# Performance work log

Hardware: AMD Instinct MI355X
Metric: run time of the kernel (lower is better)

## Reference

```python
import jax, jax.numpy as jnp
import numpy as np

L, H, D, DH, F, V, S, B, CTX = 6, 12, 768, 64, 3072, 32000, 1024, 2, 1024
EPS = 1e-5


def layernorm(x, scale, bias):
    mu = jnp.mean(x, axis=-1, keepdims=True)
    var = jnp.mean(jnp.square(x - mu), axis=-1, keepdims=True)
    return (x - mu) * jax.lax.rsqrt(var + EPS) * scale + bias


def setup_inputs() -> dict:
    key = jax.random.key(0)
    ks = jax.random.split(key, 16)
    std = 0.02
    res_std = 0.02 * (2 * L) ** (-0.5)
    inp = {
        "X": jax.random.randint(ks[0], (B, S), 0, V),
        "emb": jax.random.normal(ks[1], (V, D), jnp.float32) * std,            # tied with head weight
        "pos_emb": jax.random.normal(ks[2], (CTX, D), jnp.float32) * 0.01,
        "Wq": jax.random.normal(ks[3], (L, H, D, DH), jnp.float32) * std,
        "bq": jnp.zeros((L, H, DH), jnp.float32),
        "Wk": jax.random.normal(ks[4], (L, H, D, DH), jnp.float32) * std,
        "bk": jnp.zeros((L, H, DH), jnp.float32),
        "Wv": jax.random.normal(ks[5], (L, H, D, DH), jnp.float32) * std,
        "bv": jnp.zeros((L, H, DH), jnp.float32),
        "Wo": jax.random.normal(ks[6], (L, H * DH, D), jnp.float32) * res_std,  # ResidualScaledLinear
        "bo": jnp.zeros((L, D), jnp.float32),
        "ln1_s": jnp.ones((L, D), jnp.float32),
        "ln1_b": jnp.zeros((L, D), jnp.float32),
        "ln2_s": jnp.ones((L, D), jnp.float32),
        "ln2_b": jnp.zeros((L, D), jnp.float32),
        "W1": jax.random.normal(ks[7], (L, D, F), jnp.float32) * std,
        "b1": jnp.zeros((L, F), jnp.float32),
        "W2": jax.random.normal(ks[8], (L, F, D), jnp.float32) * res_std,       # ResidualScaledLinear
        "b2": jnp.zeros((L, D), jnp.float32),
        "lnf_s": jnp.ones((D,), jnp.float32),
        "lnf_b": jnp.zeros((D,), jnp.float32),
        "head_b": jnp.zeros((V,), jnp.float32),
    }
    return inp


def decoder_forward(X, emb, pos_emb, Wq, bq, Wk, bk, Wv, bv, Wo, bo,
                    ln1_s, ln1_b, ln2_s, ln2_b, W1, b1, W2, b2,
                    lnf_s, lnf_b, head_b):
    seq = X.shape[1]
    x = emb[X] + pos_emb[:seq]                      # [B,S,D]
    causal = jnp.tril(jnp.ones((seq, seq), bool))   # tril mask buffer
    scale = 1.0 / jnp.sqrt(jnp.float32(DH))
    for l in range(L):
        xn = layernorm(x, ln1_s[l], ln1_b[l])
        q = jnp.einsum('bsd,hdk->bhsk', xn, Wq[l]) + bq[l][None, :, None, :]
        k = jnp.einsum('bsd,hdk->bhsk', xn, Wk[l]) + bk[l][None, :, None, :]
        v = jnp.einsum('bsd,hdk->bhsk', xn, Wv[l]) + bv[l][None, :, None, :]
        scores = jnp.einsum('bhsk,bhtk->bhst', q, k) * scale
        scores = jnp.where(causal, scores, -jnp.inf)
        attn = jax.nn.softmax(scores, axis=-1)
        out = jnp.einsum('bhst,bhtk->bshk', attn, v).reshape(x.shape[0], seq, H * DH)
        x = x + out @ Wo[l] + bo[l]
        xn2 = layernorm(x, ln2_s[l], ln2_b[l])
        x = x + jax.nn.relu(xn2 @ W1[l] + b1[l]) @ W2[l] + b2[l]
    x = layernorm(x, lnf_s, lnf_b)
    return x @ emb.T + head_b                       # tied head weight


def reference(X, emb, pos_emb, Wq, bq, Wk, bk, Wv, bv, Wo, bo,
              ln1_s, ln1_b, ln2_s, ln2_b, W1, b1, W2, b2,
              lnf_s, lnf_b, head_b):
    return decoder_forward(X, emb, pos_emb, Wq, bq, Wk, bk, Wv, bv, Wo, bo,
                           ln1_s, ln1_b, ln2_s, ln2_b, W1, b1, W2, b2,
                           lnf_s, lnf_b, head_b)
```

## Files before the change

kernel.cpp:

```cpp
#include <hip/hip_runtime.h>
#include <cstdint>
#include <cstddef>

#define CL 6
#define CH 12
#define CD 768
#define CDH 64
#define CF 3072
#define CV 32000
#define CS 1024
#define CB 2
#define CM (CB*CS)
#define CQS 2304

typedef unsigned short u16;
typedef __bf16 bf16x8 __attribute__((ext_vector_type(8)));
typedef float f32x4 __attribute__((ext_vector_type(4)));

__device__ __forceinline__ float bf2f(u16 u) {
  union { unsigned int i; float f; } c; c.i = ((unsigned int)u) << 16; return c.f;
}
__device__ __forceinline__ u16 f2bf(float f) {
  union { float f; unsigned int i; } c; c.f = f;
  unsigned int lsb = (c.i >> 16) & 1u;
  c.i += 0x7fffu + lsb;
  return (u16)(c.i >> 16);
}

__device__ __forceinline__ void gload16(const u16* g, u16* l) {
  __builtin_amdgcn_global_load_lds(
      (const __attribute__((address_space(1))) void*)g,
      (__attribute__((address_space(3))) void*)l, 16, 0, 0);
}

__global__ __launch_bounds__(256) void convert_kernel(
    const float* __restrict__ src, u16* __restrict__ dst, int total)
{
  int idx = blockIdx.x * 256 + threadIdx.x;
  if (idx < total) dst[idx] = f2bf(src[idx]);
}

__global__ __launch_bounds__(256) void embed_kernel(
    const int* __restrict__ X, const float* __restrict__ emb,
    const float* __restrict__ pos, float* __restrict__ x)
{
  int idx = blockIdx.x * 256 + threadIdx.x;
  int m = idx / CD, d = idx - m * CD;
  int s = m & (CS - 1);
  x[idx] = emb[(size_t)X[m] * CD + d] + pos[s * CD + d];
}

__global__ __launch_bounds__(256) void ln_kernel(
    const float* __restrict__ x, const float* __restrict__ gs,
    const float* __restrict__ gb, u16* __restrict__ out)
{
  __shared__ float red[256];
  int row = blockIdx.x, tid = threadIdx.x;
  const float* xr = x + (size_t)row * CD;
  float s = 0.f;
  for (int i = tid; i < CD; i += 256) s += xr[i];
  red[tid] = s; __syncthreads();
  for (int st = 128; st > 0; st >>= 1) { if (tid < st) red[tid] += red[tid + st]; __syncthreads(); }
  float mu = red[0] * (1.f / CD); __syncthreads();
  float v = 0.f;
  for (int i = tid; i < CD; i += 256) { float d = xr[i] - mu; v += d * d; }
  red[tid] = v; __syncthreads();
  for (int st = 128; st > 0; st >>= 1) { if (tid < st) red[tid] += red[tid + st]; __syncthreads(); }
  float inv = rsqrtf(red[0] * (1.f / CD) + 1e-5f);
  u16* orow = out + (size_t)row * CD;
  for (int i = tid; i < CD; i += 256)
    orow[i] = f2bf((xr[i] - mu) * inv * gs[i] + gb[i]);
}

__global__ __launch_bounds__(256) void trans_kernel(
    u16* __restrict__ dst, const float* __restrict__ src, int R, int C)
{
  __shared__ float st[32][65];
  int r0 = blockIdx.x * 64, c0 = blockIdx.y * 32, bz = blockIdx.z;
  const float* s = src + (size_t)bz * R * C;
  u16* d = dst + (size_t)bz * R * C;
  int tx = threadIdx.x & 31, ty = threadIdx.x >> 5;
#pragma unroll
  for (int i = 0; i < 8; i++) {
    int r = ty + 8 * i;
    st[tx][r] = s[(size_t)(r0 + r) * C + c0 + tx];
  }
  __syncthreads();
  int j = threadIdx.x & 15, cbase = threadIdx.x >> 4;
#pragma unroll
  for (int i = 0; i < 2; i++) {
    int c = cbase + 16 * i;
    uint2 pk;
    u16* p = (u16*)&pk;
    p[0] = f2bf(st[c][4 * j + 0]);
    p[1] = f2bf(st[c][4 * j + 1]);
    p[2] = f2bf(st[c][4 * j + 2]);
    p[3] = f2bf(st[c][4 * j + 3]);
    *(uint2*)&d[(size_t)(c0 + c) * R + r0 + 4 * j] = pk;
  }
}

__global__ __launch_bounds__(256) void biaspack_kernel(
    const float* __restrict__ bq, const float* __restrict__ bk,
    const float* __restrict__ bv, float* __restrict__ dst)
{
  int idx = blockIdx.x * 256 + threadIdx.x;
  int l = idx / CQS, c = idx - l * CQS;
  float val;
  if (c < 768)       val = bq[l * 768 + c];
  else if (c < 1536) val = bk[l * 768 + c - 768];
  else               val = bv[l * 768 + c - 1536];
  dst[idx] = val;
}

template<bool RES, bool RELU, bool OUTBF>
__global__ __launch_bounds__(256) void gemm_kernel(
    const u16* __restrict__ A, const u16* __restrict__ Bt,
    const float* __restrict__ bias, const float* __restrict__ res,
    void* __restrict__ outp, int M, int N, int K)
{
  __shared__ __align__(16) u16 As[64 * 32];
  __shared__ __align__(16) u16 Bs[64 * 32];
  int tid = threadIdx.x;
  int m0 = blockIdx.y * 64, n0 = blockIdx.x * 64;
  int wid = tid >> 6, lane = tid & 63;
  int quad = lane >> 4, l16 = lane & 15;
  int wm = (wid >> 1) * 32, wn = (wid & 1) * 32;
  int r = tid >> 2, c8 = (tid & 3) * 8;

  f32x4 zero = {0.f, 0.f, 0.f, 0.f};
  f32x4 acc[2][2];
  acc[0][0] = zero; acc[0][1] = zero; acc[1][0] = zero; acc[1][1] = zero;

  for (int kt = 0; kt < K; kt += 32) {
    uint4 av = *(const uint4*)(A  + (size_t)(m0 + r) * K + kt + c8);
    uint4 bv = *(const uint4*)(Bt + (size_t)(n0 + r) * K + kt + c8);
    __syncthreads();
    *(uint4*)&As[r * 32 + c8] = av;
    *(uint4*)&Bs[r * 32 + c8] = bv;
    __syncthreads();
    bf16x8 af[2], bfr[2];
#pragma unroll
    for (int i = 0; i < 2; i++) {
      af[i]  = *reinterpret_cast<const bf16x8*>(&As[(wm + i * 16 + l16) * 32 + quad * 8]);
      bfr[i] = *reinterpret_cast<const bf16x8*>(&Bs[(wn + i * 16 + l16) * 32 + quad * 8]);
    }
#pragma unroll
    for (int i = 0; i < 2; i++)
#pragma unroll
      for (int j = 0; j < 2; j++)
        acc[i][j] = __builtin_amdgcn_mfma_f32_16x16x32_bf16(af[i], bfr[j], acc[i][j], 0, 0, 0);
  }

#pragma unroll
  for (int i = 0; i < 2; i++) {
    int gmb = m0 + wm + i * 16 + quad * 4;
#pragma unroll
    for (int j = 0; j < 2; j++) {
      int gn = n0 + wn + j * 16 + l16;
      float bsv = bias[gn];
#pragma unroll
      for (int rr = 0; rr < 4; rr++) {
        float val = acc[i][j][rr] + bsv;
        if (RELU) val = fmaxf(val, 0.f);
        size_t o = (size_t)(gmb + rr) * N + gn;
        if (RES) val += res[o];
        if (OUTBF) ((u16*)outp)[o] = f2bf(val);
        else       ((float*)outp)[o] = val;
      }
    }
  }
}

template<bool RES, bool RELU, bool OUTBF>
__global__ __launch_bounds__(256) void gemm128_kernel(
    const u16* __restrict__ A, const u16* __restrict__ Bt,
    const float* __restrict__ bias, const float* __restrict__ res,
    void* __restrict__ outp, int M, int N, int K)
{
  __shared__ __align__(16) u16 As[128 * 32];
  __shared__ __align__(16) u16 Bs[128 * 32];
  int tid = threadIdx.x;
  int nbm = M >> 7, nbn = N >> 7, nwg = nbm * nbn;
  int orig = blockIdx.x;
  int q8 = nwg >> 3, r8 = nwg & 7;
  int xcd = orig & 7;
  int t = ((xcd < r8) ? xcd * (q8 + 1) : r8 * (q8 + 1) + (xcd - r8) * q8) + (orig >> 3);
  int bm = t % nbm, bn = t / nbm;
  int m0 = bm << 7, n0 = bn << 7;

  int wv = tid >> 6, ln = tid & 63;
  int quad = ln >> 4, l16 = ln & 15;
  int wr = wv >> 1, wc = wv & 1;

  int srow = wv * 16 + (ln >> 2);
  int scol = (ln & 3) * 8;
  const u16* ga0 = A  + (size_t)(m0 + srow) * K + scol;
  const u16* ga1 = A  + (size_t)(m0 + srow + 64) * K + scol;
  const u16* gb0 = Bt + (size_t)(n0 + srow) * K + scol;
  const u16* gb1 = Bt + (size_t)(n0 + srow + 64) * K + scol;
  u16* lA0 = As + wv * 512;
  u16* lA1 = As + 2048 + wv * 512;
  u16* lB0 = Bs + wv * 512;
  u16* lB1 = Bs + 2048 + wv * 512;

  f32x4 acc[4][4];
#pragma unroll
  for (int i = 0; i < 4; i++)
#pragma unroll
    for (int j = 0; j < 4; j++) acc[i][j] = f32x4{0.f, 0.f, 0.f, 0.f};

  for (int kt = 0; kt < K; kt += 32) {
    __syncthreads();
    gload16(ga0 + kt, lA0);
    gload16(ga1 + kt, lA1);
    gload16(gb0 + kt, lB0);
    gload16(gb1 + kt, lB1);
    __syncthreads();
    bf16x8 af[4], bf[4];
#pragma unroll
    for (int i = 0; i < 4; i++)
      af[i] = *reinterpret_cast<const bf16x8*>(&As[(wr * 64 + i * 16 + l16) * 32 + quad * 8]);
#pragma unroll
    for (int j = 0; j < 4; j++)
      bf[j] = *reinterpret_cast<const bf16x8*>(&Bs[(wc * 64 + j * 16 + l16) * 32 + quad * 8]);
#pragma unroll
    for (int i = 0; i < 4; i++)
#pragma unroll
      for (int j = 0; j < 4; j++)
        acc[i][j] = __builtin_amdgcn_mfma_f32_16x16x32_bf16(af[i], bf[j], acc[i][j], 0, 0, 0);
  }

#pragma unroll
  for (int i = 0; i < 4; i++) {
    int gm = m0 + wr * 64 + i * 16 + quad * 4;
#pragma unroll
    for (int j = 0; j < 4; j++) {
      int gn = n0 + wc * 64 + j * 16 + l16;
      float bsv = bias[gn];
#pragma unroll
      for (int rr = 0; rr < 4; rr++) {
        float val = acc[i][j][rr] + bsv;
        if (RELU) val = fmaxf(val, 0.f);
        size_t oo = (size_t)(gm + rr) * N + gn;
        if (RES) val += res[oo];
        if (OUTBF) ((u16*)outp)[oo] = f2bf(val);
        else       ((float*)outp)[oo] = val;
      }
    }
  }
}

__global__ __launch_bounds__(256) void attn_mfma_kernel(
    const u16* __restrict__ qkv, u16* __restrict__ o)
{
  __shared__ __align__(16) u16 Ks[64 * 64];
  __shared__ __align__(16) u16 Vt[64 * 64];
  __shared__ __align__(16) u16 Ps[4 * 16 * 64];

  int tid = threadIdx.x;
  int qb = (CS / 64 - 1) - blockIdx.x;
  int h = blockIdx.y, b = blockIdx.z;
  int wid = tid >> 6, lane = tid & 63, quad = lane >> 4, l16 = lane & 15;
  int q0 = qb * 64;
  size_t bh = (size_t)b * CS * CQS + h * CDH;

  bf16x8 aq[2];
  {
    const u16* qrow = qkv + bh + (size_t)(q0 + wid * 16 + l16) * CQS;
#pragma unroll
    for (int ks = 0; ks < 2; ks++) {
      uint4 t = *(const uint4*)(qrow + ks * 32 + quad * 8);
      aq[ks] = *reinterpret_cast<bf16x8*>(&t);
    }
  }

  f32x4 oacc[4];
  float mrow[4], lrow[4];
#pragma unroll
  for (int j = 0; j < 4; j++) oacc[j] = f32x4{0.f, 0.f, 0.f, 0.f};
#pragma unroll
  for (int r = 0; r < 4; r++) { mrow[r] = -1e30f; lrow[r] = 0.f; }

  int srow = tid >> 3, schunk = tid & 7;
  int vrow = tid >> 2, vseg = (tid & 3) * 16;

  for (int t0 = 0; t0 <= q0; t0 += 64) {
    __syncthreads();
#pragma unroll
    for (int it = 0; it < 2; it++) {
      int row = srow + it * 32;
      uint4 kv4 = *(const uint4*)(qkv + bh + 768 + (size_t)(t0 + row) * CQS + schunk * 8);
      *(uint4*)&Ks[row * 64 + ((schunk ^ (row & 7)) * 8)] = kv4;
    }
    {
      const u16* vr = qkv + bh + 1536 + (size_t)(t0 + vrow) * CQS + vseg;
      uint4 a0 = *(const uint4*)(vr);
      uint4 a1 = *(const uint4*)(vr + 8);
      int c = vrow >> 3, w7 = vrow & 7;
#pragma unroll
      for (int i = 0; i < 16; i++) {
        int d = vseg + i;
        u16 val = (i < 8) ? ((const u16*)&a0)[i] : ((const u16*)&a1)[i - 8];
        Vt[d * 64 + (((c ^ (d & 7)) * 8) | w7)] = val;
      }
    }
    __syncthreads();

    f32x4 sacc[4];
#pragma unroll
    for (int j = 0; j < 4; j++) sacc[j] = f32x4{0.f, 0.f, 0.f, 0.f};
#pragma unroll
    for (int j = 0; j < 4; j++) {
      int row = j * 16 + l16;
#pragma unroll
      for (int ks = 0; ks < 2; ks++) {
        bf16x8 bk = *reinterpret_cast<const bf16x8*>(
            &Ks[row * 64 + ((((ks * 4 + quad) ^ (row & 7)) * 8))]);
        sacc[j] = __builtin_amdgcn_mfma_f32_16x16x32_bf16(aq[ks], bk, sacc[j], 0, 0, 0);
      }
    }

    int qg0 = q0 + wid * 16 + quad * 4;
#pragma unroll
    for (int j = 0; j < 4; j++) {
      int tg = t0 + j * 16 + l16;
#pragma unroll
      for (int r = 0; r < 4; r++) {
        float s = sacc[j][r] * 0.125f;
        sacc[j][r] = (tg <= qg0 + r) ? s : -1e30f;
      }
    }

#pragma unroll
    for (int r = 0; r < 4; r++) {
      float m = fmaxf(fmaxf(sacc[0][r], sacc[1][r]), fmaxf(sacc[2][r], sacc[3][r]));
#pragma unroll
      for (int sh = 1; sh < 16; sh <<= 1) m = fmaxf(m, __shfl_xor(m, sh, 64));
      float mnew = fmaxf(mrow[r], m);
      float scal = __expf(mrow[r] - mnew);
      mrow[r] = mnew;
      lrow[r] *= scal;
#pragma unroll
      for (int j = 0; j < 4; j++) oacc[j][r] *= scal;
      float sum = 0.f;
#pragma unroll
      for (int j = 0; j < 4; j++) {
        float p = __expf(sacc[j][r] - mnew);
        sacc[j][r] = p;
        sum += p;
      }
#pragma unroll
      for (int sh = 1; sh < 16; sh <<= 1) sum += __shfl_xor(sum, sh, 64);
      lrow[r] += sum;
    }

    u16* Pw = Ps + wid * 1024;
#pragma unroll
    for (int j = 0; j < 4; j++) {
      int c = (l16 >> 3) + 2 * j;
#pragma unroll
      for (int r = 0; r < 4; r++) {
        int row = quad * 4 + r;
        Pw[row * 64 + (((c ^ (row & 7)) * 8) | (l16 & 7))] = f2bf(sacc[j][r]);
      }
    }

    bf16x8 ap[2];
#pragma unroll
    for (int ks = 0; ks < 2; ks++)
      ap[ks] = *reinterpret_cast<const bf16x8*>(
          &Pw[l16 * 64 + ((((ks * 4 + quad) ^ (l16 & 7)) * 8))]);
#pragma unroll
    for (int j = 0; j < 4; j++) {
      int row = j * 16 + l16;
#pragma unroll
      for (int ks = 0; ks < 2; ks++) {
        bf16x8 bv = *reinterpret_cast<const bf16x8*>(
            &Vt[row * 64 + ((((ks * 4 + quad) ^ (row & 7)) * 8))]);
        oacc[j] = __builtin_amdgcn_mfma_f32_16x16x32_bf16(ap[ks], bv, oacc[j], 0, 0, 0);
      }
    }
  }

#pragma unroll
  for (int r = 0; r < 4; r++) {
    float inv = 1.f / lrow[r];
    int qg = q0 + wid * 16 + quad * 4 + r;
    u16* orow = o + (size_t)b * CS * CD + h * CDH + (size_t)qg * CD;
#pragma unroll
    for (int j = 0; j < 4; j++)
      orow[j * 16 + l16] = f2bf(oacc[j][r] * inv);
  }
}

extern "C" void kernel_launch(void* const* d_in, const int* in_sizes, int n_in,
                              void* d_out, int out_size, void* d_ws, size_t ws_size,
                              hipStream_t stream) {
  const int*   X      = (const int*)d_in[0];
  const float* emb    = (const float*)d_in[1];
  const float* pos    = (const float*)d_in[2];
  const float* Wq     = (const float*)d_in[3];
  const float* bq     = (const float*)d_in[4];
  const float* Wk     = (const float*)d_in[5];
  const float* bk     = (const float*)d_in[6];
  const float* Wv     = (const float*)d_in[7];
  const float* bv     = (const float*)d_in[8];
  const float* Wo     = (const float*)d_in[9];
  const float* bo     = (const float*)d_in[10];
  const float* ln1s   = (const float*)d_in[11];
  const float* ln1b   = (const float*)d_in[12];
  const float* ln2s   = (const float*)d_in[13];
  const float* ln2b   = (const float*)d_in[14];
  const float* W1     = (const float*)d_in[15];
  const float* b1     = (const float*)d_in[16];
  const float* W2     = (const float*)d_in[17];
  const float* b2     = (const float*)d_in[18];
  const float* lnfs   = (const float*)d_in[19];
  const float* lnfb   = (const float*)d_in[20];
  const float* headb  = (const float*)d_in[21];
  (void)in_sizes; (void)n_in; (void)out_size; (void)ws_size;

  char* ws = (char*)d_ws;
  size_t off = 0;
  auto alloc = [&](size_t bytes) { void* p = ws + off; off += (bytes + 255) & ~(size_t)255; return p; };

  float* x     = (float*)alloc((size_t)CM * CD * 4);
  u16*   xn    = (u16*)  alloc((size_t)CM * CD * 2);
  u16*   qkvb  = (u16*)  alloc((size_t)CM * CQS * 2);
  u16*   ao    = (u16*)  alloc((size_t)CM * CD * 2);
  u16*   hb    = (u16*)  alloc((size_t)CM * CF * 2);
  u16*   Wqkvt = (u16*)  alloc((size_t)CQS * CD * 2);
  u16*   Wot   = (u16*)  alloc((size_t)CD * CD * 2);
  u16*   W1t   = (u16*)  alloc((size_t)CD * CF * 2);
  u16*   W2t   = (u16*)  alloc((size_t)CD * CF * 2);
  u16*   embC  = (u16*)  alloc((size_t)CV * CD * 2);
  float* biasp = (float*)alloc((size_t)CL * CQS * 4);

  embed_kernel<<<CM * CD / 256, 256, 0, stream>>>(X, emb, pos, x);
  convert_kernel<<<(CV * CD) / 256, 256, 0, stream>>>(emb, embC, CV * CD);
  biaspack_kernel<<<(CL * CQS) / 256, 256, 0, stream>>>(bq, bk, bv, biasp);

  const int QKV_TOT = CH * CD * CDH;
  const int OO_TOT  = CD * CD;
  const int FF_TOT  = CD * CF;

  for (int l = 0; l < CL; l++) {
    trans_kernel<<<dim3(CD / 64, CDH / 32, CH), 256, 0, stream>>>(Wqkvt,                 Wq + (size_t)l * QKV_TOT, CD, CDH);
    trans_kernel<<<dim3(CD / 64, CDH / 32, CH), 256, 0, stream>>>(Wqkvt + 768 * 768,     Wk + (size_t)l * QKV_TOT, CD, CDH);
    trans_kernel<<<dim3(CD / 64, CDH / 32, CH), 256, 0, stream>>>(Wqkvt + 1536 * 768,    Wv + (size_t)l * QKV_TOT, CD, CDH);
    trans_kernel<<<dim3(CD / 64, CD / 32, 1),   256, 0, stream>>>(Wot, Wo + (size_t)l * OO_TOT, CD, CD);
    trans_kernel<<<dim3(CD / 64, CF / 32, 1),   256, 0, stream>>>(W1t, W1 + (size_t)l * FF_TOT, CD, CF);
    trans_kernel<<<dim3(CF / 64, CD / 32, 1),   256, 0, stream>>>(W2t, W2 + (size_t)l * FF_TOT, CF, CD);

    ln_kernel<<<CM, 256, 0, stream>>>(x, ln1s + l * CD, ln1b + l * CD, xn);

    gemm128_kernel<false, false, true><<<(CM / 128) * (CQS / 128), 256, 0, stream>>>(
        xn, Wqkvt, biasp + l * CQS, nullptr, qkvb, CM, CQS, CD);

    attn_mfma_kernel<<<dim3(CS / 64, CH, CB), 256, 0, stream>>>(qkvb, ao);

    gemm_kernel<true, false, false><<<dim3(CD / 64, CM / 64), 256, 0, stream>>>(ao, Wot, bo + l * CD, x, x, CM, CD, CD);

    ln_kernel<<<CM, 256, 0, stream>>>(x, ln2s + l * CD, ln2b + l * CD, xn);

    gemm128_kernel<false, true, true><<<(CM / 128) * (CF / 128), 256, 0, stream>>>(
        xn, W1t, b1 + l * CF, nullptr, hb, CM, CF, CD);

    gemm_kernel<true, false, false><<<dim3(CD / 64, CM / 64), 256, 0, stream>>>(hb, W2t, b2 + l * CD, x, x, CM, CD, CF);
  }

  ln_kernel<<<CM, 256, 0, stream>>>(x, lnfs, lnfb, xn);
  gemm128_kernel<false, false, false><<<(CM / 128) * (CV / 128), 256, 0, stream>>>(
      xn, embC, headb, nullptr, d_out, CM, CV, CD);
}
```

Measured before the change: 1.656 ms.

## Deepen GEMM K-tiles to 64, batch weight transposes, and use shuffle-based layernorm

```diff
diff --git a/kernel.cpp b/kernel.cpp
--- a/kernel.cpp
+++ b/kernel.cpp
@@ -54,31 +54,38 @@
     const float* __restrict__ x, const float* __restrict__ gs,
     const float* __restrict__ gb, u16* __restrict__ out)
 {
-  __shared__ float red[256];
+  __shared__ float rs[4], rss[4];
   int row = blockIdx.x, tid = threadIdx.x;
   const float* xr = x + (size_t)row * CD;
-  float s = 0.f;
-  for (int i = tid; i < CD; i += 256) s += xr[i];
-  red[tid] = s; __syncthreads();
-  for (int st = 128; st > 0; st >>= 1) { if (tid < st) red[tid] += red[tid + st]; __syncthreads(); }
-  float mu = red[0] * (1.f / CD); __syncthreads();
-  float v = 0.f;
-  for (int i = tid; i < CD; i += 256) { float d = xr[i] - mu; v += d * d; }
-  red[tid] = v; __syncthreads();
-  for (int st = 128; st > 0; st >>= 1) { if (tid < st) red[tid] += red[tid + st]; __syncthreads(); }
-  float inv = rsqrtf(red[0] * (1.f / CD) + 1e-5f);
+  float a0 = xr[tid], a1 = xr[tid + 256], a2 = xr[tid + 512];
+  float s = a0 + a1 + a2;
+  float ss = a0 * a0 + a1 * a1 + a2 * a2;
+#pragma unroll
+  for (int sh = 32; sh > 0; sh >>= 1) {
+    s  += __shfl_xor(s, sh, 64);
+    ss += __shfl_xor(ss, sh, 64);
+  }
+  int w = tid >> 6;
+  if ((tid & 63) == 0) { rs[w] = s; rss[w] = ss; }
+  __syncthreads();
+  s  = rs[0] + rs[1] + rs[2] + rs[3];
+  ss = rss[0] + rss[1] + rss[2] + rss[3];
+  float mu = s * (1.f / CD);
+  float inv = rsqrtf(ss * (1.f / CD) - mu * mu + 1e-5f);
   u16* orow = out + (size_t)row * CD;
-  for (int i = tid; i < CD; i += 256)
-    orow[i] = f2bf((xr[i] - mu) * inv * gs[i] + gb[i]);
+  orow[tid]       = f2bf((a0 - mu) * inv * gs[tid]       + gb[tid]);
+  orow[tid + 256] = f2bf((a1 - mu) * inv * gs[tid + 256] + gb[tid + 256]);
+  orow[tid + 512] = f2bf((a2 - mu) * inv * gs[tid + 512] + gb[tid + 512]);
 }
 
 __global__ __launch_bounds__(256) void trans_kernel(
-    u16* __restrict__ dst, const float* __restrict__ src, int R, int C)
+    u16* __restrict__ dst, const float* __restrict__ src, int R, int C,
+    int PB, long dstL)
 {
   __shared__ float st[32][65];
   int r0 = blockIdx.x * 64, c0 = blockIdx.y * 32, bz = blockIdx.z;
   const float* s = src + (size_t)bz * R * C;
-  u16* d = dst + (size_t)bz * R * C;
+  u16* d = dst + (size_t)(bz / PB) * dstL + (size_t)(bz % PB) * R * C;
   int tx = threadIdx.x & 31, ty = threadIdx.x >> 5;
 #pragma unroll
   for (int i = 0; i < 8; i++) {
@@ -114,42 +121,50 @@
 }
 
 template<bool RES, bool RELU, bool OUTBF>
-__global__ __launch_bounds__(256) void gemm_kernel(
+__global__ __launch_bounds__(256) void gemm64v2_kernel(
     const u16* __restrict__ A, const u16* __restrict__ Bt,
     const float* __restrict__ bias, const float* __restrict__ res,
     void* __restrict__ outp, int M, int N, int K)
 {
-  __shared__ __align__(16) u16 As[64 * 32];
-  __shared__ __align__(16) u16 Bs[64 * 32];
+  __shared__ __align__(16) u16 As[64 * 64];
+  __shared__ __align__(16) u16 Bs[64 * 64];
   int tid = threadIdx.x;
   int m0 = blockIdx.y * 64, n0 = blockIdx.x * 64;
-  int wid = tid >> 6, lane = tid & 63;
-  int quad = lane >> 4, l16 = lane & 15;
-  int wm = (wid >> 1) * 32, wn = (wid & 1) * 32;
-  int r = tid >> 2, c8 = (tid & 3) * 8;
-
-  f32x4 zero = {0.f, 0.f, 0.f, 0.f};
+  int wv = tid >> 6, ln = tid & 63;
+  int quad = ln >> 4, l16 = ln & 15;
+  int wm = (wv >> 1) * 32, wn = (wv & 1) * 32;
+
+  int srow = wv * 8 + (ln >> 3);
+  int scol = (ln & 7) * 8;
+  const u16* gA = A  + (size_t)(m0 + srow) * K + scol;
+  const u16* gB = Bt + (size_t)(n0 + srow) * K + scol;
+
   f32x4 acc[2][2];
-  acc[0][0] = zero; acc[0][1] = zero; acc[1][0] = zero; acc[1][1] = zero;
-
-  for (int kt = 0; kt < K; kt += 32) {
-    uint4 av = *(const uint4*)(A  + (size_t)(m0 + r) * K + kt + c8);
-    uint4 bv = *(const uint4*)(Bt + (size_t)(n0 + r) * K + kt + c8);
+  acc[0][0] = f32x4{0,0,0,0}; acc[0][1] = f32x4{0,0,0,0};
+  acc[1][0] = f32x4{0,0,0,0}; acc[1][1] = f32x4{0,0,0,0};
+
+  for (int kt = 0; kt < K; kt += 64) {
     __syncthreads();
-    *(uint4*)&As[r * 32 + c8] = av;
-    *(uint4*)&Bs[r * 32 + c8] = bv;
+#pragma unroll
+    for (int it = 0; it < 2; it++) {
+      gload16(gA + (size_t)it * 32 * K + kt, As + it * 2048 + wv * 512);
+      gload16(gB + (size_t)it * 32 * K + kt, Bs + it * 2048 + wv * 512);
+    }
     __syncthreads();
-    bf16x8 af[2], bfr[2];
-#pragma unroll
-    for (int i = 0; i < 2; i++) {
-      af[i]  = *reinterpret_cast<const bf16x8*>(&As[(wm + i * 16 + l16) * 32 + quad * 8]);
-      bfr[i] = *reinterpret_cast<const bf16x8*>(&Bs[(wn + i * 16 + l16) * 32 + quad * 8]);
-    }
-#pragma unroll
-    for (int i = 0; i < 2; i++)
-#pragma unroll
-      for (int j = 0; j < 2; j++)
-        acc[i][j] = __builtin_amdgcn_mfma_f32_16x16x32_bf16(af[i], bfr[j], acc[i][j], 0, 0, 0);
+#pragma unroll
+    for (int h = 0; h < 2; h++) {
+      bf16x8 af[2], bf[2];
+#pragma unroll
+      for (int i = 0; i < 2; i++) {
+        af[i] = *reinterpret_cast<const bf16x8*>(&As[(wm + i * 16 + l16) * 64 + h * 32 + quad * 8]);
+        bf[i] = *reinterpret_cast<const bf16x8*>(&Bs[(wn + i * 16 + l16) * 64 + h * 32 + quad * 8]);
+      }
+#pragma unroll
+      for (int i = 0; i < 2; i++)
+#pragma unroll
+        for (int j = 0; j < 2; j++)
+          acc[i][j] = __builtin_amdgcn_mfma_f32_16x16x32_bf16(af[i], bf[j], acc[i][j], 0, 0, 0);
+    }
   }
 
 #pragma unroll
@@ -178,8 +193,8 @@
     const float* __restrict__ bias, const float* __restrict__ res,
     void* __restrict__ outp, int M, int N, int K)
 {
-  __shared__ __align__(16) u16 As[128 * 32];
-  __shared__ __align__(16) u16 Bs[128 * 32];
+  __shared__ __align__(16) u16 As[128 * 64];
+  __shared__ __align__(16) u16 Bs[128 * 64];
   int tid = threadIdx.x;
   int nbm = M >> 7, nbn = N >> 7, nwg = nbm * nbn;
   int orig = blockIdx.x;
@@ -193,16 +208,10 @@
   int quad = ln >> 4, l16 = ln & 15;
   int wr = wv >> 1, wc = wv & 1;
 
-  int srow = wv * 16 + (ln >> 2);
-  int scol = (ln & 3) * 8;
-  const u16* ga0 = A  + (size_t)(m0 + srow) * K + scol;
-  const u16* ga1 = A  + (size_t)(m0 + srow + 64) * K + scol;
-  const u16* gb0 = Bt + (size_t)(n0 + srow) * K + scol;
-  const u16* gb1 = Bt + (size_t)(n0 + srow + 64) * K + scol;
-  u16* lA0 = As + wv * 512;
-  u16* lA1 = As + 2048 + wv * 512;
-  u16* lB0 = Bs + wv * 512;
-  u16* lB1 = Bs + 2048 + wv * 512;
+  int srow = wv * 8 + (ln >> 3);
+  int scol = (ln & 7) * 8;
+  const u16* gA = A  + (size_t)(m0 + srow) * K + scol;
+  const u16* gB = Bt + (size_t)(n0 + srow) * K + scol;
 
   f32x4 acc[4][4];
 #pragma unroll
@@ -210,25 +219,29 @@
 #pragma unroll
     for (int j = 0; j < 4; j++) acc[i][j] = f32x4{0.f, 0.f, 0.f, 0.f};
 
-  for (int kt = 0; kt < K; kt += 32) {
+  for (int kt = 0; kt < K; kt += 64) {
     __syncthreads();
-    gload16(ga0 + kt, lA0);
-    gload16(ga1 + kt, lA1);
-    gload16(gb0 + kt, lB0);
-    gload16(gb1 + kt, lB1);
+#pragma unroll
+    for (int it = 0; it < 4; it++) {
+      gload16(gA + (size_t)it * 32 * K + kt, As + it * 2048 + wv * 512);
+      gload16(gB + (size_t)it * 32 * K + kt, Bs + it * 2048 + wv * 512);
+    }
     __syncthreads();
-    bf16x8 af[4], bf[4];
-#pragma unroll
-    for (int i = 0; i < 4; i++)
-      af[i] = *reinterpret_cast<const bf16x8*>(&As[(wr * 64 + i * 16 + l16) * 32 + quad * 8]);
-#pragma unroll
-    for (int j = 0; j < 4; j++)
-      bf[j] = *reinterpret_cast<const bf16x8*>(&Bs[(wc * 64 + j * 16 + l16) * 32 + quad * 8]);
-#pragma unroll
-    for (int i = 0; i < 4; i++)
+#pragma unroll
+    for (int h = 0; h < 2; h++) {
+      bf16x8 af[4], bf[4];
+#pragma unroll
+      for (int i = 0; i < 4; i++)
+        af[i] = *reinterpret_cast<const bf16x8*>(&As[(wr * 64 + i * 16 + l16) * 64 + h * 32 + quad * 8]);
 #pragma unroll
       for (int j = 0; j < 4; j++)
-        acc[i][j] = __builtin_amdgcn_mfma_f32_16x16x32_bf16(af[i], bf[j], acc[i][j], 0, 0, 0);
+        bf[j] = *reinterpret_cast<const bf16x8*>(&Bs[(wc * 64 + j * 16 + l16) * 64 + h * 32 + quad * 8]);
+#pragma unroll
+      for (int i = 0; i < 4; i++)
+#pragma unroll
+        for (int j = 0; j < 4; j++)
+          acc[i][j] = __builtin_amdgcn_mfma_f32_16x16x32_bf16(af[i], bf[j], acc[i][j], 0, 0, 0);
+    }
   }
 
 #pragma unroll
@@ -419,7 +432,7 @@
   const float* lnfs   = (const float*)d_in[19];
   const float* lnfb   = (const float*)d_in[20];
   const float* headb  = (const float*)d_in[21];
-  (void)in_sizes; (void)n_in; (void)out_size; (void)ws_size;
+  (void)in_sizes; (void)n_in; (void)out_size;
 
   char* ws = (char*)d_ws;
   size_t off = 0;
@@ -430,44 +443,67 @@
   u16*   qkvb  = (u16*)  alloc((size_t)CM * CQS * 2);
   u16*   ao    = (u16*)  alloc((size_t)CM * CD * 2);
   u16*   hb    = (u16*)  alloc((size_t)CM * CF * 2);
-  u16*   Wqkvt = (u16*)  alloc((size_t)CQS * CD * 2);
-  u16*   Wot   = (u16*)  alloc((size_t)CD * CD * 2);
-  u16*   W1t   = (u16*)  alloc((size_t)CD * CF * 2);
-  u16*   W2t   = (u16*)  alloc((size_t)CD * CF * 2);
   u16*   embC  = (u16*)  alloc((size_t)CV * CD * 2);
   float* biasp = (float*)alloc((size_t)CL * CQS * 4);
+
+  const size_t WQKV = (size_t)CQS * CD;
+  const size_t WOO  = (size_t)CD * CD;
+  const size_t WFF  = (size_t)CD * CF;
+  size_t perLayerElems = WQKV + WOO + 2 * WFF;
+  bool fused = (ws_size >= off + (size_t)CL * perLayerElems * 2 + 4096);
+  int LW = fused ? CL : 1;
+  u16* Wqkvt = (u16*)alloc((size_t)LW * WQKV * 2);
+  u16* Wot   = (u16*)alloc((size_t)LW * WOO * 2);
+  u16* W1t   = (u16*)alloc((size_t)LW * WFF * 2);
+  u16* W2t   = (u16*)alloc((size_t)LW * WFF * 2);
 
   embed_kernel<<<CM * CD / 256, 256, 0, stream>>>(X, emb, pos, x);
   convert_kernel<<<(CV * CD) / 256, 256, 0, stream>>>(emb, embC, CV * CD);
   biaspack_kernel<<<(CL * CQS) / 256, 256, 0, stream>>>(bq, bk, bv, biasp);
 
+  if (fused) {
+    trans_kernel<<<dim3(CD / 64, CDH / 32, CL * CH), 256, 0, stream>>>(Wqkvt,              Wq, CD, CDH, CH, (long)WQKV);
+    trans_kernel<<<dim3(CD / 64, CDH / 32, CL * CH), 256, 0, stream>>>(Wqkvt + 768 * 768,  Wk, CD, CDH, CH, (long)WQKV);
+    trans_kernel<<<dim3(CD / 64, CDH / 32, CL * CH), 256, 0, stream>>>(Wqkvt + 1536 * 768, Wv, CD, CDH, CH, (long)WQKV);
+    trans_kernel<<<dim3(CD / 64, CD / 32, CL), 256, 0, stream>>>(Wot, Wo, CD, CD, 1, (long)WOO);
+    trans_kernel<<<dim3(CD / 64, CF / 32, CL), 256, 0, stream>>>(W1t, W1, CD, CF, 1, (long)WFF);
+    trans_kernel<<<dim3(CF / 64, CD / 32, CL), 256, 0, stream>>>(W2t, W2, CF, CD, 1, (long)WFF);
+  }
+
   const int QKV_TOT = CH * CD * CDH;
-  const int OO_TOT  = CD * CD;
-  const int FF_TOT  = CD * CF;
 
   for (int l = 0; l < CL; l++) {
-    trans_kernel<<<dim3(CD / 64, CDH / 32, CH), 256, 0, stream>>>(Wqkvt,                 Wq + (size_t)l * QKV_TOT, CD, CDH);
-    trans_kernel<<<dim3(CD / 64, CDH / 32, CH), 256, 0, stream>>>(Wqkvt + 768 * 768,     Wk + (size_t)l * QKV_TOT, CD, CDH);
-    trans_kernel<<<dim3(CD / 64, CDH / 32, CH), 256, 0, stream>>>(Wqkvt + 1536 * 768,    Wv + (size_t)l * QKV_TOT, CD, CDH);
-    trans_kernel<<<dim3(CD / 64, CD / 32, 1),   256, 0, stream>>>(Wot, Wo + (size_t)l * OO_TOT, CD, CD);
-    trans_kernel<<<dim3(CD / 64, CF / 32, 1),   256, 0, stream>>>(W1t, W1 + (size_t)l * FF_TOT, CD, CF);
-    trans_kernel<<<dim3(CF / 64, CD / 32, 1),   256, 0, stream>>>(W2t, W2 + (size_t)l * FF_TOT, CF, CD);
+    if (!fused) {
+      trans_kernel<<<dim3(CD / 64, CDH / 32, CH), 256, 0, stream>>>(Wqkvt,              Wq + (size_t)l * QKV_TOT, CD, CDH, CH, (long)WQKV);
+      trans_kernel<<<dim3(CD / 64, CDH / 32, CH), 256, 0, stream>>>(Wqkvt + 768 * 768,  Wk + (size_t)l * QKV_TOT, CD, CDH, CH, (long)WQKV);
+      trans_kernel<<<dim3(CD / 64, CDH / 32, CH), 256, 0, stream>>>(Wqkvt + 1536 * 768, Wv + (size_t)l * QKV_TOT, CD, CDH, CH, (long)WQKV);
+      trans_kernel<<<dim3(CD / 64, CD / 32, 1), 256, 0, stream>>>(Wot, Wo + (size_t)l * WOO, CD, CD, 1, (long)WOO);
+      trans_kernel<<<dim3(CD / 64, CF / 32, 1), 256, 0, stream>>>(W1t, W1 + (size_t)l * WFF, CD, CF, 1, (long)WFF);
+      trans_kernel<<<dim3(CF / 64, CD / 32, 1), 256, 0, stream>>>(W2t, W2 + (size_t)l * WFF, CF, CD, 1, (long)WFF);
+    }
+    int lw = fused ? l : 0;
+    const u16* wqkv = Wqkvt + (size_t)lw * WQKV;
+    const u16* wot  = Wot   + (size_t)lw * WOO;
+    const u16* w1t  = W1t   + (size_t)lw * WFF;
+    const u16* w2t  = W2t   + (size_t)lw * WFF;
 
     ln_kernel<<<CM, 256, 0, stream>>>(x, ln1s + l * CD, ln1b + l * CD, xn);
 
     gemm128_kernel<false, false, true><<<(CM / 128) * (CQS / 128), 256, 0, stream>>>(
-        xn, Wqkvt, biasp + l * CQS, nullptr, qkvb, CM, CQS, CD);
+        xn, wqkv, biasp + l * CQS, nullptr, qkvb, CM, CQS, CD);
 
     attn_mfma_kernel<<<dim3(CS / 64, CH, CB), 256, 0, stream>>>(qkvb, ao);
 
-    gemm_kernel<true, false, false><<<dim3(CD / 64, CM / 64), 256, 0, stream>>>(ao, Wot, bo + l * CD, x, x, CM, CD, CD);
+    gemm64v2_kernel<true, false, false><<<dim3(CD / 64, CM / 64), 256, 0, stream>>>(
+        ao, wot, bo + l * CD, x, x, CM, CD, CD);
 
     ln_kernel<<<CM, 256, 0, stream>>>(x, ln2s + l * CD, ln2b + l * CD, xn);
 
     gemm128_kernel<false, true, true><<<(CM / 128) * (CF / 128), 256, 0, stream>>>(
-        xn, W1t, b1 + l * CF, nullptr, hb, CM, CF, CD);
-
-    gemm_kernel<true, false, false><<<dim3(CD / 64, CM / 64), 256, 0, stream>>>(hb, W2t, b2 + l * CD, x, x, CM, CD, CF);
+        xn, w1t, b1 + l * CF, nullptr, hb, CM, CF, CD);
+
+    gemm64v2_kernel<true, false, false><<<dim3(CD / 64, CM / 64), 256, 0, stream>>>(
+        hb, w2t, b2 + l * CD, x, x, CM, CD, CF);
   }
 
   ln_kernel<<<CM, 256, 0, stream>>>(x, lnfs, lnfb, xn);
```

Measured after the change: 1.579 ms. -4.6%, faster.
